# Kernel optimization log

Hardware: AMD Instinct MI355X
Metric: run time of the kernel (lower is better)

The kernel has to match this reference:

```python
import jax, jax.numpy as jnp
import numpy as np

G, N, E, B = 4, 50000, 800000, 32
F_IN, H, HEADS, NUM_NODES = 64, 128, 8, 50000
HD = H // HEADS
LO, HI = 50.0, 110.0


def setup_inputs() -> dict:
    key = jax.random.key(0)
    ks = jax.random.split(key, 10)
    x = jax.random.normal(ks[0], (G, N, F_IN), jnp.float32)
    edge_index = jax.random.randint(ks[1], (G, 2, E), 0, N)
    batch = jnp.sort(jax.random.randint(ks[2], (G, N), 0, B), axis=-1)
    init = lambda k, shape, fan: (jax.random.normal(k, shape, jnp.float32) / np.sqrt(fan)).astype(jnp.float32)
    W1 = init(ks[3], (F_IN, H), F_IN); b1 = jnp.zeros((H,), jnp.float32)
    W2 = init(ks[4], (H, H), H);       b2 = jnp.zeros((H,), jnp.float32)
    in_proj_w = init(ks[5], (3 * H, H), H); in_proj_b = jnp.zeros((3 * H,), jnp.float32)
    out_proj_w = init(ks[6], (H, H), H);    out_proj_b = jnp.zeros((H,), jnp.float32)
    lin_w = init(ks[7], (NUM_NODES, H), H); lin_b = jnp.zeros((NUM_NODES,), jnp.float32)
    return dict(x=x, edge_index=edge_index, batch=batch, W1=W1, b1=b1, W2=W2, b2=b2,
                in_proj_w=in_proj_w, in_proj_b=in_proj_b, out_proj_w=out_proj_w,
                out_proj_b=out_proj_b, lin_w=lin_w, lin_b=lin_b)


def _gcn(x, row, col, W, b):
    # PyG GCNConv: add self-loops, sym-normalized scatter-add aggregation.
    h = x @ W  # [N,H]
    deg = jax.ops.segment_sum(jnp.ones((E,), x.dtype), col, num_segments=N) + 1.0  # +1 self-loop
    dinv = jax.lax.rsqrt(deg)
    norm = dinv[row] * dinv[col]  # [E]
    agg = jax.ops.segment_sum(h[row] * norm[:, None], col, num_segments=N)
    agg = agg + h * (1.0 / deg)[:, None]  # self-loop message (norm = 1/deg)
    return agg + b


def _per_graph(xg, eig, bg, W1, b1, W2, b2):
    row, col = eig[0], eig[1]
    h = jax.nn.relu(_gcn(xg, row, col, W1, b1))
    h = jax.nn.relu(_gcn(h, row, col, W2, b2))
    s = jax.ops.segment_sum(h, bg, num_segments=B)  # [B,H]
    cnt = jax.ops.segment_sum(jnp.ones((N,), h.dtype), bg, num_segments=B)
    return jnp.where(cnt[:, None] > 0, s / jnp.maximum(cnt, 1.0)[:, None], 0.0)


def reference(x, edge_index, batch, W1, b1, W2, b2, in_proj_w, in_proj_b,
              out_proj_w, out_proj_b, lin_w, lin_b):
    # per-graph GCN + mean pool -> embeddings [G, B, H] (seq-first for torch MHA)
    emb = jax.vmap(_per_graph, in_axes=(0, 0, 0, None, None, None, None))(
        x, edge_index, batch, W1, b1, W2, b2)
    # torch MultiheadAttention (self-attention, seq-first)
    q = emb @ in_proj_w[:H].T + in_proj_b[:H]
    k = emb @ in_proj_w[H:2 * H].T + in_proj_b[H:2 * H]
    v = emb @ in_proj_w[2 * H:].T + in_proj_b[2 * H:]
    qh = q.reshape(G, B, HEADS, HD)
    kh = k.reshape(G, B, HEADS, HD)
    vh = v.reshape(G, B, HEADS, HD)
    scores = jnp.einsum('gbhd,kbhd->bhgk', qh, kh) / np.sqrt(HD)
    attn = jax.nn.softmax(scores, axis=-1)
    ctx = jnp.einsum('bhgk,kbhd->gbhd', attn, vh).reshape(G, B, H)
    attended = ctx @ out_proj_w.T + out_proj_b  # [G,B,H]
    pooled = attended.mean(axis=1)  # [G,H]
    out = pooled @ lin_w.T + lin_b  # [G,NUM_NODES]
    return out * (HI - LO) + LO
```

## Files before the change

### kernel.cpp

```cpp
#include <hip/hip_runtime.h>

#define Gn 4
#define Nn 50000
#define En 800000
#define Bq 32
#define F_IN 64
#define Hn 128
#define NNODES 50000
#define NBK 196
#define EB 98

using v8s = __attribute__((ext_vector_type(8))) short;
using v4f = __attribute__((ext_vector_type(4))) float;

__device__ __forceinline__ float bf2f(unsigned short u) {
    unsigned int x = ((unsigned int)u) << 16;
    float f; __builtin_memcpy(&f, &x, 4); return f;
}
__device__ __forceinline__ unsigned short f2bf(float f) {
    unsigned int x; __builtin_memcpy(&x, &f, 4);
    x = (x + 0x7fffu + ((x >> 16) & 1u)) >> 16;
    return (unsigned short)x;
}

__global__ __launch_bounds__(256) void k_btot(const int* __restrict__ ei, int* __restrict__ btot) {
    __shared__ int h[NBK];
    int g = blockIdx.y;
    const int* col = ei + (size_t)g * 2 * En + En;
    for (int i = threadIdx.x; i < NBK; i += 256) h[i] = 0;
    __syncthreads();
    int e0 = blockIdx.x * 8192, e1 = min(e0 + 8192, En);
    for (int i = e0 / 4 + threadIdx.x; i < e1 / 4; i += 256) {
        int4 c = ((const int4*)col)[i];
        atomicAdd(&h[c.x >> 8], 1);
        atomicAdd(&h[c.y >> 8], 1);
        atomicAdd(&h[c.z >> 8], 1);
        atomicAdd(&h[c.w >> 8], 1);
    }
    __syncthreads();
    for (int i = threadIdx.x; i < NBK; i += 256)
        if (h[i]) atomicAdd(&btot[g * NBK + i], h[i]);
}

__global__ __launch_bounds__(256) void k_bbase(const int* __restrict__ btot, int* __restrict__ bbase,
                                               int* __restrict__ bcur) {
    __shared__ int s[256];
    int g = blockIdx.x, t = threadIdx.x;
    int v = (t < NBK) ? btot[g * NBK + t] : 0;
    s[t] = v;
    __syncthreads();
    for (int d = 1; d < 256; d <<= 1) {
        int u = (t >= d) ? s[t - d] : 0;
        __syncthreads();
        s[t] += u;
        __syncthreads();
    }
    if (t < NBK) { int b = s[t] - v; bbase[g * NBK + t] = b; bcur[g * NBK + t] = b; }
}

__global__ __launch_bounds__(256) void k_bucket(const int* __restrict__ ei, int* __restrict__ bcur,
                                                unsigned int* __restrict__ pairs) {
    __shared__ int h[NBK];
    __shared__ int gbase[NBK];
    int g = blockIdx.y;
    const int* row = ei + (size_t)g * 2 * En;
    const int* col = row + En;
    unsigned int* pg = pairs + (size_t)g * En;
    for (int i = threadIdx.x; i < NBK; i += 256) h[i] = 0;
    __syncthreads();
    int e0 = blockIdx.x * 8192, e1 = min(e0 + 8192, En);
    for (int i = e0 / 4 + threadIdx.x; i < e1 / 4; i += 256) {
        int4 c = ((const int4*)col)[i];
        atomicAdd(&h[c.x >> 8], 1);
        atomicAdd(&h[c.y >> 8], 1);
        atomicAdd(&h[c.z >> 8], 1);
        atomicAdd(&h[c.w >> 8], 1);
    }
    __syncthreads();
    for (int i = threadIdx.x; i < NBK; i += 256) {
        int cnt = h[i];
        gbase[i] = cnt ? atomicAdd(&bcur[g * NBK + i], cnt) : 0;
        h[i] = 0;
    }
    __syncthreads();
    for (int i = e0 / 4 + threadIdx.x; i < e1 / 4; i += 256) {
        int4 c = ((const int4*)col)[i];
        int4 r = ((const int4*)row)[i];
        int p;
        p = gbase[c.x >> 8] + atomicAdd(&h[c.x >> 8], 1); pg[p] = ((unsigned)r.x << 16) | (unsigned)c.x;
        p = gbase[c.y >> 8] + atomicAdd(&h[c.y >> 8], 1); pg[p] = ((unsigned)r.y << 16) | (unsigned)c.y;
        p = gbase[c.z >> 8] + atomicAdd(&h[c.z >> 8], 1); pg[p] = ((unsigned)r.z << 16) | (unsigned)c.z;
        p = gbase[c.w >> 8] + atomicAdd(&h[c.w >> 8], 1); pg[p] = ((unsigned)r.w << 16) | (unsigned)c.w;
    }
}

__global__ __launch_bounds__(256) void k_fillb2(const unsigned int* __restrict__ pairs,
                                                const int* __restrict__ bbase, const int* __restrict__ btot,
                                                int* __restrict__ off, float* __restrict__ dinv,
                                                unsigned short* __restrict__ srcs) {
    __shared__ int h[256], sc[256], curL[256];
    int g = blockIdx.y, b = blockIdx.x, t = threadIdx.x;
    int beg = bbase[g * NBK + b], cnt = btot[g * NBK + b];
    const unsigned int* pg = pairs + (size_t)g * En + beg;
    unsigned short* sg = srcs + (size_t)g * En;
    h[t] = 0;
    __syncthreads();
    for (int i = t; i < cnt; i += 256) atomicAdd(&h[pg[i] & 255], 1);
    __syncthreads();
    int d = h[t];
    sc[t] = d;
    __syncthreads();
    for (int dd = 1; dd < 256; dd <<= 1) {
        int u = (t >= dd) ? sc[t - dd] : 0;
        __syncthreads();
        sc[t] += u;
        __syncthreads();
    }
    int myoff = beg + sc[t] - d;
    int node = b * 256 + t;
    if (node < Nn) {
        off[g * (Nn + 1) + node] = myoff;
        dinv[g * Nn + node] = rsqrtf((float)d + 1.0f);
    }
    if (b == NBK - 1 && t == 255) off[g * (Nn + 1) + Nn] = beg + sc[255];
    curL[t] = myoff;
    __syncthreads();
    for (int i = t; i < cnt; i += 256) {
        unsigned int pr = pg[i];
        int pos = atomicAdd(&curL[pr & 255], 1);
        sg[pos] = (unsigned short)(pr >> 16);
    }
}

__global__ __launch_bounds__(256) void k_cast(const float* __restrict__ x, const float* __restrict__ dinv,
                                              unsigned short* __restrict__ xbs) {
    int g = blockIdx.y;
    int i = blockIdx.x * 256 + threadIdx.x;
    if (i >= Nn * 16) return;
    float dc = dinv[g * Nn + (i >> 4)];
    float4 v = *(const float4*)&x[(size_t)g * Nn * 64 + i * 4];
    ushort4 u = make_ushort4(f2bf(v.x * dc), f2bf(v.y * dc), f2bf(v.z * dc), f2bf(v.w * dc));
    *(ushort4*)&xbs[(size_t)g * Nn * 64 + i * 4] = u;
}

__global__ __launch_bounds__(256) void k_agg1(const unsigned short* __restrict__ xs_, const int* __restrict__ off_,
                                              const unsigned short* __restrict__ srcs_,
                                              const float* __restrict__ dinv_, unsigned short* __restrict__ z1_) {
    int g = blockIdx.y;
    const unsigned short* xs = xs_ + (size_t)g * Nn * 64;
    const int* off = off_ + g * (Nn + 1);
    const unsigned short* srcs = srcs_ + (size_t)g * En;
    unsigned short* z1 = z1_ + (size_t)g * Nn * 64;
    int node = blockIdx.x * 8 + (threadIdx.x >> 5);
    int lane = threadIdx.x & 31;
    int sub = lane >> 3;
    int fo = lane & 7;
    int beg = off[node], end = off[node + 1];
    float acc[8] = {};
    for (int e = beg; e < end; e += 32) {
        int rem = end - e;
        int sj[8];
#pragma unroll
        for (int jj = 0; jj < 8; ++jj) sj[jj] = srcs[e + jj * 4 + sub];
#pragma unroll
        for (int jj = 0; jj < 8; ++jj) {
            if (jj * 4 + sub < rem) {
                v8s u = *(const v8s*)&xs[(long)sj[jj] * 64 + fo * 8];
#pragma unroll
                for (int q = 0; q < 8; ++q) acc[q] += bf2f((unsigned short)u[q]);
            }
        }
    }
#pragma unroll
    for (int q = 0; q < 8; ++q) {
        acc[q] += __shfl_xor(acc[q], 8, 32);
        acc[q] += __shfl_xor(acc[q], 16, 32);
    }
    if (sub == 0) {
        float dc = dinv_[g * Nn + node];
        v8s ow = *(const v8s*)&xs[(long)node * 64 + fo * 8];
        ushort4 o0, o1;
        o0.x = f2bf((acc[0] + bf2f((unsigned short)ow[0])) * dc);
        o0.y = f2bf((acc[1] + bf2f((unsigned short)ow[1])) * dc);
        o0.z = f2bf((acc[2] + bf2f((unsigned short)ow[2])) * dc);
        o0.w = f2bf((acc[3] + bf2f((unsigned short)ow[3])) * dc);
        o1.x = f2bf((acc[4] + bf2f((unsigned short)ow[4])) * dc);
        o1.y = f2bf((acc[5] + bf2f((unsigned short)ow[5])) * dc);
        o1.z = f2bf((acc[6] + bf2f((unsigned short)ow[6])) * dc);
        o1.w = f2bf((acc[7] + bf2f((unsigned short)ow[7])) * dc);
        *(ushort4*)&z1[(long)node * 64 + fo * 8] = o0;
        *(ushort4*)&z1[(long)node * 64 + fo * 8 + 4] = o1;
    }
}

__global__ __launch_bounds__(256) void k_agg2(const unsigned short* __restrict__ h_, const int* __restrict__ off_,
                                              const unsigned short* __restrict__ srcs_,
                                              const float* __restrict__ dinv_, unsigned short* __restrict__ z2_) {
    int g = blockIdx.y;
    const unsigned short* h = h_ + (size_t)g * Nn * 128;
    const int* off = off_ + g * (Nn + 1);
    const unsigned short* srcs = srcs_ + (size_t)g * En;
    unsigned short* z2 = z2_ + (size_t)g * Nn * 128;
    int node = blockIdx.x * 8 + (threadIdx.x >> 5);
    int lane = threadIdx.x & 31;
    int sub = lane >> 3;
    int fo = lane & 7;
    int beg = off[node], end = off[node + 1];
    float acc[16] = {};
    for (int e = beg; e < end; e += 32) {
        int rem = end - e;
        int sj[8];
#pragma unroll
        for (int jj = 0; jj < 8; ++jj) sj[jj] = srcs[e + jj * 4 + sub];
#pragma unroll
        for (int jj = 0; jj < 8; ++jj) {
            if (jj * 4 + sub < rem) {
                const unsigned short* rp = &h[(long)sj[jj] * 128 + fo * 16];
                v8s u0 = *(const v8s*)rp;
                v8s u1 = *(const v8s*)(rp + 8);
#pragma unroll
                for (int q = 0; q < 8; ++q) acc[q] += bf2f((unsigned short)u0[q]);
#pragma unroll
                for (int q = 0; q < 8; ++q) acc[8 + q] += bf2f((unsigned short)u1[q]);
            }
        }
    }
#pragma unroll
    for (int q = 0; q < 16; ++q) {
        acc[q] += __shfl_xor(acc[q], 8, 32);
        acc[q] += __shfl_xor(acc[q], 16, 32);
    }
    if (sub == 0) {
        float dc = dinv_[g * Nn + node];
        const unsigned short* op = &h[(long)node * 128 + fo * 16];
        unsigned short* zp = &z2[(long)node * 128 + fo * 16];
#pragma unroll
        for (int q4 = 0; q4 < 4; ++q4) {
            ushort4 ow = *(const ushort4*)(op + q4 * 4);
            ushort4 o;
            o.x = f2bf((acc[q4 * 4 + 0] + bf2f(ow.x)) * dc);
            o.y = f2bf((acc[q4 * 4 + 1] + bf2f(ow.y)) * dc);
            o.z = f2bf((acc[q4 * 4 + 2] + bf2f(ow.z)) * dc);
            o.w = f2bf((acc[q4 * 4 + 3] + bf2f(ow.w)) * dc);
            *(ushort4*)(zp + q4 * 4) = o;
        }
    }
}

template <int K, bool SCALE>
__global__ __launch_bounds__(256) void k_mmfma(const unsigned short* __restrict__ zin_,
                                               const float* __restrict__ W, const float* __restrict__ bias,
                                               const float* __restrict__ dinv_,
                                               unsigned short* __restrict__ outp_) {
    __shared__ __align__(16) unsigned short Wt[128 * (K + 8)];
    __shared__ __align__(16) unsigned short At[32 * (K + 8)];
    int g = blockIdx.y;
    const unsigned short* zin = zin_ + (size_t)g * Nn * K;
    const float* dinv = dinv_ + g * Nn;
    unsigned short* outp = outp_ + (size_t)g * Nn * 128;
    int t = threadIdx.x;
    int base = blockIdx.x * 32;

#pragma unroll
    for (int i = 0; i < K * 128 / 256; ++i) {
        int idx = i * 256 + t;
        int k = idx >> 7, n = idx & 127;
        Wt[n * (K + 8) + k] = f2bf(W[idx]);
    }
    {
        int r = t >> 3, cb = (t & 7) * (K / 8);
        long grow = base + r;
#pragma unroll
        for (int j = 0; j < K / 32; ++j) {
            ushort4 u = make_ushort4(0, 0, 0, 0);
            if (grow < Nn) u = *(const ushort4*)&zin[grow * K + cb + j * 4];
            *(ushort4*)&At[r * (K + 8) + cb + j * 4] = u;
        }
    }
    __syncthreads();

    int w = t >> 6, lane = t & 63;
    int wm = w & 1, wn = w >> 1;
    int m = lane & 15, q = lane >> 4;
    v4f acc[4] = {};
    const unsigned short* Ap = &At[(wm * 16 + m) * (K + 8) + q * 8];
    const unsigned short* Bp = &Wt[(wn * 64 + m) * (K + 8) + q * 8];
    const int rstep = 16 * (K + 8);
#pragma unroll
    for (int ks = 0; ks < K / 32; ++ks) {
        v8s a = *(const v8s*)(Ap + ks * 32);
        v8s b0 = *(const v8s*)(Bp + 0 * rstep + ks * 32);
        v8s b1 = *(const v8s*)(Bp + 1 * rstep + ks * 32);
        v8s b2 = *(const v8s*)(Bp + 2 * rstep + ks * 32);
        v8s b3 = *(const v8s*)(Bp + 3 * rstep + ks * 32);
        acc[0] = __builtin_amdgcn_mfma_f32_16x16x32_bf16(a, b0, acc[0], 0, 0, 0);
        acc[1] = __builtin_amdgcn_mfma_f32_16x16x32_bf16(a, b1, acc[1], 0, 0, 0);
        acc[2] = __builtin_amdgcn_mfma_f32_16x16x32_bf16(a, b2, acc[2], 0, 0, 0);
        acc[3] = __builtin_amdgcn_mfma_f32_16x16x32_bf16(a, b3, acc[3], 0, 0, 0);
    }

    int col0 = wn * 64 + m;
    int rbase = base + wm * 16 + q * 4;
    float dv[4];
#pragma unroll
    for (int rg = 0; rg < 4; ++rg)
        dv[rg] = SCALE ? ((rbase + rg < Nn) ? dinv[rbase + rg] : 1.f) : 1.f;
#pragma unroll
    for (int nt = 0; nt < 4; ++nt) {
        float bc = bias[col0 + nt * 16];
#pragma unroll
        for (int rg = 0; rg < 4; ++rg) {
            int row = rbase + rg;
            if (row < Nn) {
                float o = fmaxf(acc[nt][rg] + bc, 0.f);
                outp[(long)row * 128 + col0 + nt * 16] = f2bf(o * dv[rg]);
            }
        }
    }
}

__global__ __launch_bounds__(128) void k_pool(const unsigned short* __restrict__ y_, const int* __restrict__ bat,
                                              float* __restrict__ emb_sum, float* __restrict__ cnt) {
    int g = blockIdx.y;
    const unsigned short* y = y_ + (size_t)g * Nn * 128;
    const int* batch = bat + (size_t)g * Nn;
    int f = threadIdx.x;
    int start = blockIdx.x * 64;
    int end = min(start + 64, Nn);
    if (start >= Nn) return;
    float acc = 0.f;
    int cacc = 0;
    int cur = batch[start];
    for (int i = start; i < end; ++i) {
        int b = batch[i];
        if (b != cur) {
            atomicAdd(&emb_sum[(g * Bq + cur) * Hn + f], acc);
            if (f == 0) atomicAdd(&cnt[g * Bq + cur], (float)cacc);
            acc = 0.f; cacc = 0; cur = b;
        }
        acc += bf2f(y[(long)i * Hn + f]);
        cacc++;
    }
    atomicAdd(&emb_sum[(g * Bq + cur) * Hn + f], acc);
    if (f == 0) atomicAdd(&cnt[g * Bq + cur], (float)cacc);
}

__global__ __launch_bounds__(128) void k_attn(const float* __restrict__ emb_sum, const float* __restrict__ cnt,
                                              const float* __restrict__ ipw, const float* __restrict__ ipb,
                                              const float* __restrict__ opw, const float* __restrict__ opb,
                                              float* __restrict__ pooled) {
    int b = blockIdx.x;
    int f = threadIdx.x;
    __shared__ float es[4][128], qs[4][128], ks[4][128], vs[4][128], sc[128], cx[4][128];
#pragma unroll
    for (int g = 0; g < 4; ++g) {
        float c = cnt[g * Bq + b];
        es[g][f] = (c > 0.f) ? emb_sum[(g * Bq + b) * Hn + f] / c : 0.f;
    }
    __syncthreads();
#pragma unroll
    for (int g = 0; g < 4; ++g) {
        float q = ipb[f], k = ipb[Hn + f], v = ipb[2 * Hn + f];
        for (int j = 0; j < Hn; ++j) {
            float e = es[g][j];
            q += e * ipw[f * Hn + j];
            k += e * ipw[(Hn + f) * Hn + j];
            v += e * ipw[(2 * Hn + f) * Hn + j];
        }
        qs[g][f] = q; ks[g][f] = k; vs[g][f] = v;
    }
    __syncthreads();
    {
        int h = f >> 4, g = (f >> 2) & 3, kk = f & 3;
        float s = 0.f;
        for (int d = 0; d < 16; ++d) s += qs[g][h * 16 + d] * ks[kk][h * 16 + d];
        sc[f] = s * 0.25f;
    }
    __syncthreads();
    {
        int h = f >> 4;
#pragma unroll
        for (int g = 0; g < 4; ++g) {
            int bi = h * 16 + g * 4;
            float s0 = sc[bi], s1 = sc[bi + 1], s2 = sc[bi + 2], s3 = sc[bi + 3];
            float m = fmaxf(fmaxf(s0, s1), fmaxf(s2, s3));
            float e0 = __expf(s0 - m), e1 = __expf(s1 - m), e2 = __expf(s2 - m), e3 = __expf(s3 - m);
            float rinv = 1.f / (e0 + e1 + e2 + e3);
            cx[g][f] = (e0 * vs[0][f] + e1 * vs[1][f] + e2 * vs[2][f] + e3 * vs[3][f]) * rinv;
        }
    }
    __syncthreads();
#pragma unroll
    for (int g = 0; g < 4; ++g) {
        float a = opb[f];
        for (int j = 0; j < Hn; ++j) a += cx[g][j] * opw[f * Hn + j];
        atomicAdd(&pooled[g * Hn + f], a * (1.0f / Bq));
    }
}

__global__ __launch_bounds__(256) void k_final(const float* __restrict__ pooled, const float* __restrict__ lw,
                                               const float* __restrict__ lb, float* __restrict__ out) {
    __shared__ float ps[512];
    int t = threadIdx.x;
    ps[t] = pooled[t];
    ps[t + 256] = pooled[t + 256];
    __syncthreads();
    int wave = t >> 6, lane = t & 63;
    int n = blockIdx.x * 4 + wave;
    if (n >= NNODES) return;
    float2 w = *(const float2*)&lw[(long)n * 128 + lane * 2];
    float a0 = w.x * ps[0 * 128 + lane * 2] + w.y * ps[0 * 128 + lane * 2 + 1];
    float a1 = w.x * ps[1 * 128 + lane * 2] + w.y * ps[1 * 128 + lane * 2 + 1];
    float a2 = w.x * ps[2 * 128 + lane * 2] + w.y * ps[2 * 128 + lane * 2 + 1];
    float a3 = w.x * ps[3 * 128 + lane * 2] + w.y * ps[3 * 128 + lane * 2 + 1];
#pragma unroll
    for (int off = 32; off > 0; off >>= 1) {
        a0 += __shfl_down(a0, off);
        a1 += __shfl_down(a1, off);
        a2 += __shfl_down(a2, off);
        a3 += __shfl_down(a3, off);
    }
    if (lane == 0) {
        float bn = lb[n];
        out[0 * NNODES + n] = (a0 + bn) * 60.f + 50.f;
        out[1 * NNODES + n] = (a1 + bn) * 60.f + 50.f;
        out[2 * NNODES + n] = (a2 + bn) * 60.f + 50.f;
        out[3 * NNODES + n] = (a3 + bn) * 60.f + 50.f;
    }
}

extern "C" void kernel_launch(void* const* d_in, const int* in_sizes, int n_in,
                              void* d_out, int out_size, void* d_ws, size_t ws_size,
                              hipStream_t stream) {
    const float* x   = (const float*)d_in[0];
    const int*   ei  = (const int*)d_in[1];
    const int*   bat = (const int*)d_in[2];
    const float* W1  = (const float*)d_in[3];
    const float* b1  = (const float*)d_in[4];
    const float* W2  = (const float*)d_in[5];
    const float* b2  = (const float*)d_in[6];
    const float* ipw = (const float*)d_in[7];
    const float* ipb = (const float*)d_in[8];
    const float* opw = (const float*)d_in[9];
    const float* opb = (const float*)d_in[10];
    const float* lw  = (const float*)d_in[11];
    const float* lb  = (const float*)d_in[12];
    float* out = (float*)d_out;

    char* p = (char*)d_ws;
    unsigned short* xbs = (unsigned short*)p;
    unsigned short* z1  = (unsigned short*)(p + 25600000);
    unsigned short* y1b = (unsigned short*)(p + 51200000);
    unsigned short* z2  = (unsigned short*)(p + 102400000);
    unsigned int*   pairs = (unsigned int*)(p + 102400000);
    unsigned short* y2b = (unsigned short*)(p + 153600000);
    char* meta = p + 204800000;
    int*   off  = (int*)meta;
    float* dinv = (float*)(off + 4 * (Nn + 1));
    int*   btot  = (int*)(dinv + 4 * Nn);
    int*   bbase = btot + 4 * NBK;
    int*   bcur  = bbase + 4 * NBK;
    unsigned short* srcs = (unsigned short*)(bcur + 4 * NBK);
    float* emb    = (float*)(srcs + (size_t)4 * En);
    float* cnt    = emb + Gn * Bq * Hn;
    float* pooled = cnt + Gn * Bq;

    hipMemsetAsync(btot, 0, 4 * NBK * sizeof(int), stream);
    hipMemsetAsync(emb, 0, Gn * Bq * Hn * sizeof(float), stream);
    hipMemsetAsync(cnt, 0, Gn * Bq * sizeof(float), stream);
    hipMemsetAsync(pooled, 0, Gn * Hn * sizeof(float), stream);

    const int agGrid = (Nn + 7) / 8;
    const int mmGrid = (Nn + 31) / 32;
    const int plGrid = (Nn + 63) / 64;
    const int ctGrid = (Nn * 16 + 255) / 256;

    k_btot<<<dim3(EB, Gn), 256, 0, stream>>>(ei, btot);
    k_bbase<<<Gn, 256, 0, stream>>>(btot, bbase, bcur);
    k_bucket<<<dim3(EB, Gn), 256, 0, stream>>>(ei, bcur, pairs);
    k_fillb2<<<dim3(NBK, Gn), 256, 0, stream>>>(pairs, bbase, btot, off, dinv, srcs);

    k_cast<<<dim3(ctGrid, Gn), 256, 0, stream>>>(x, dinv, xbs);
    k_agg1<<<dim3(agGrid, Gn), 256, 0, stream>>>(xbs, off, srcs, dinv, z1);
    k_mmfma<64, true><<<dim3(mmGrid, Gn), 256, 0, stream>>>(z1, W1, b1, dinv, y1b);
    k_agg2<<<dim3(agGrid, Gn), 256, 0, stream>>>(y1b, off, srcs, dinv, z2);
    k_mmfma<128, false><<<dim3(mmGrid, Gn), 256, 0, stream>>>(z2, W2, b2, dinv, y2b);
    k_pool<<<dim3(plGrid, Gn), 128, 0, stream>>>(y2b, bat, emb, cnt);

    k_attn<<<Bq, 128, 0, stream>>>(emb, cnt, ipw, ipb, opw, opb, pooled);
    k_final<<<(NNODES + 3) / 4, 256, 0, stream>>>(pooled, lw, lb, out);
}
```

Before: 527.5 us.

## Reuse per-block column histograms and software-pipeline neighbor gathers in aggregation

k_btot now stores each block's column-bucket histogram to workspace, so k_bucket reads it instead of recounting the column array. The aggregation kernels replace the 32-edge batched gather with a loop that prefetches the next neighbor row and index one step ahead, using clamped indices and a multiplicative mask instead of branches. This cuts a redundant read of the edge columns and aims to hide gather latency. In exchange, the aggregation loop now has a serial dependency with only one load in flight per lane, and each padded step does masked work.

```diff
diff --git a/kernel.cpp b/kernel.cpp
--- a/kernel.cpp
+++ b/kernel.cpp
@@ -23,7 +23,8 @@
     return (unsigned short)x;
 }
 
-__global__ __launch_bounds__(256) void k_btot(const int* __restrict__ ei, int* __restrict__ btot) {
+__global__ __launch_bounds__(256) void k_btot(const int* __restrict__ ei, int* __restrict__ btot,
+                                              int* __restrict__ chist) {
     __shared__ int h[NBK];
     int g = blockIdx.y;
     const int* col = ei + (size_t)g * 2 * En + En;
@@ -38,8 +39,12 @@
         atomicAdd(&h[c.w >> 8], 1);
     }
     __syncthreads();
-    for (int i = threadIdx.x; i < NBK; i += 256)
-        if (h[i]) atomicAdd(&btot[g * NBK + i], h[i]);
+    int* ch = chist + ((size_t)g * EB + blockIdx.x) * NBK;
+    for (int i = threadIdx.x; i < NBK; i += 256) {
+        int v = h[i];
+        ch[i] = v;
+        if (v) atomicAdd(&btot[g * NBK + i], v);
+    }
 }
 
 __global__ __launch_bounds__(256) void k_bbase(const int* __restrict__ btot, int* __restrict__ bbase,
@@ -59,30 +64,22 @@
 }
 
 __global__ __launch_bounds__(256) void k_bucket(const int* __restrict__ ei, int* __restrict__ bcur,
-                                                unsigned int* __restrict__ pairs) {
+                                                unsigned int* __restrict__ pairs,
+                                                const int* __restrict__ chist) {
     __shared__ int h[NBK];
     __shared__ int gbase[NBK];
     int g = blockIdx.y;
     const int* row = ei + (size_t)g * 2 * En;
     const int* col = row + En;
     unsigned int* pg = pairs + (size_t)g * En;
-    for (int i = threadIdx.x; i < NBK; i += 256) h[i] = 0;
-    __syncthreads();
-    int e0 = blockIdx.x * 8192, e1 = min(e0 + 8192, En);
-    for (int i = e0 / 4 + threadIdx.x; i < e1 / 4; i += 256) {
-        int4 c = ((const int4*)col)[i];
-        atomicAdd(&h[c.x >> 8], 1);
-        atomicAdd(&h[c.y >> 8], 1);
-        atomicAdd(&h[c.z >> 8], 1);
-        atomicAdd(&h[c.w >> 8], 1);
-    }
-    __syncthreads();
+    const int* ch = chist + ((size_t)g * EB + blockIdx.x) * NBK;
     for (int i = threadIdx.x; i < NBK; i += 256) {
-        int cnt = h[i];
+        int cnt = ch[i];
         gbase[i] = cnt ? atomicAdd(&bcur[g * NBK + i], cnt) : 0;
         h[i] = 0;
     }
     __syncthreads();
+    int e0 = blockIdx.x * 8192, e1 = min(e0 + 8192, En);
     for (int i = e0 / 4 + threadIdx.x; i < e1 / 4; i += 256) {
         int4 c = ((const int4*)col)[i];
         int4 r = ((const int4*)row)[i];
@@ -156,20 +153,20 @@
     int sub = lane >> 3;
     int fo = lane & 7;
     int beg = off[node], end = off[node + 1];
+    int d = end - beg;
+    int dm1 = max(d - 1, 0);
+    int nst = (d + 3) >> 2;
     float acc[8] = {};
-    for (int e = beg; e < end; e += 32) {
-        int rem = end - e;
-        int sj[8];
-#pragma unroll
-        for (int jj = 0; jj < 8; ++jj) sj[jj] = srcs[e + jj * 4 + sub];
-#pragma unroll
-        for (int jj = 0; jj < 8; ++jj) {
-            if (jj * 4 + sub < rem) {
-                v8s u = *(const v8s*)&xs[(long)sj[jj] * 64 + fo * 8];
-#pragma unroll
-                for (int q = 0; q < 8; ++q) acc[q] += bf2f((unsigned short)u[q]);
-            }
-        }
+    int sb = srcs[beg + min(sub, dm1)];
+    v8s c = *(const v8s*)&xs[(long)sb * 64 + fo * 8];
+    sb = srcs[beg + min(4 + sub, dm1)];
+    for (int st = 0; st < nst; ++st) {
+        v8s n = *(const v8s*)&xs[(long)sb * 64 + fo * 8];
+        sb = srcs[beg + min((st + 2) * 4 + sub, dm1)];
+        float m = (st * 4 + sub < d) ? 1.f : 0.f;
+#pragma unroll
+        for (int q = 0; q < 8; ++q) acc[q] += m * bf2f((unsigned short)c[q]);
+        c = n;
     }
 #pragma unroll
     for (int q = 0; q < 8; ++q) {
@@ -206,24 +203,26 @@
     int sub = lane >> 3;
     int fo = lane & 7;
     int beg = off[node], end = off[node + 1];
+    int d = end - beg;
+    int dm1 = max(d - 1, 0);
+    int nst = (d + 3) >> 2;
     float acc[16] = {};
-    for (int e = beg; e < end; e += 32) {
-        int rem = end - e;
-        int sj[8];
-#pragma unroll
-        for (int jj = 0; jj < 8; ++jj) sj[jj] = srcs[e + jj * 4 + sub];
-#pragma unroll
-        for (int jj = 0; jj < 8; ++jj) {
-            if (jj * 4 + sub < rem) {
-                const unsigned short* rp = &h[(long)sj[jj] * 128 + fo * 16];
-                v8s u0 = *(const v8s*)rp;
-                v8s u1 = *(const v8s*)(rp + 8);
-#pragma unroll
-                for (int q = 0; q < 8; ++q) acc[q] += bf2f((unsigned short)u0[q]);
-#pragma unroll
-                for (int q = 0; q < 8; ++q) acc[8 + q] += bf2f((unsigned short)u1[q]);
-            }
-        }
+    int sb = srcs[beg + min(sub, dm1)];
+    const unsigned short* rp = &h[(long)sb * 128 + fo * 16];
+    v8s c0 = *(const v8s*)rp;
+    v8s c1 = *(const v8s*)(rp + 8);
+    sb = srcs[beg + min(4 + sub, dm1)];
+    for (int st = 0; st < nst; ++st) {
+        const unsigned short* rpn = &h[(long)sb * 128 + fo * 16];
+        v8s n0 = *(const v8s*)rpn;
+        v8s n1 = *(const v8s*)(rpn + 8);
+        sb = srcs[beg + min((st + 2) * 4 + sub, dm1)];
+        float m = (st * 4 + sub < d) ? 1.f : 0.f;
+#pragma unroll
+        for (int q = 0; q < 8; ++q) acc[q] += m * bf2f((unsigned short)c0[q]);
+#pragma unroll
+        for (int q = 0; q < 8; ++q) acc[8 + q] += m * bf2f((unsigned short)c1[q]);
+        c0 = n0; c1 = n1;
     }
 #pragma unroll
     for (int q = 0; q < 16; ++q) {
@@ -453,6 +452,7 @@
     unsigned short* y1b = (unsigned short*)(p + 51200000);
     unsigned short* z2  = (unsigned short*)(p + 102400000);
     unsigned int*   pairs = (unsigned int*)(p + 102400000);
+    int* chist = (int*)(p + 102400000 + (size_t)4 * En * 4);
     unsigned short* y2b = (unsigned short*)(p + 153600000);
     char* meta = p + 204800000;
     int*   off  = (int*)meta;
@@ -475,9 +475,9 @@
     const int plGrid = (Nn + 63) / 64;
     const int ctGrid = (Nn * 16 + 255) / 256;
 
-    k_btot<<<dim3(EB, Gn), 256, 0, stream>>>(ei, btot);
+    k_btot<<<dim3(EB, Gn), 256, 0, stream>>>(ei, btot, chist);
     k_bbase<<<Gn, 256, 0, stream>>>(btot, bbase, bcur);
-    k_bucket<<<dim3(EB, Gn), 256, 0, stream>>>(ei, bcur, pairs);
+    k_bucket<<<dim3(EB, Gn), 256, 0, stream>>>(ei, bcur, pairs, chist);
     k_fillb2<<<dim3(NBK, Gn), 256, 0, stream>>>(pairs, bbase, btot, off, dinv, srcs);
 
     k_cast<<<dim3(ctGrid, Gn), 256, 0, stream>>>(x, dinv, xbs);
```

After: 526.7 us. No clear change (-0.2%).
